# Kernel optimization log

Measured on AMD Instinct MI355X. Metric: run time of the kernel, lower is better.

## Reference

```python
import jax, jax.numpy as jnp
import numpy as np


def setup_inputs() -> dict:
    key = jax.random.key(0)
    k_idx, k_val = jax.random.split(key)
    XSIZE = 128
    N = 500000
    B = 16
    indices = jax.random.randint(k_idx, (N, 3), 0, XSIZE, dtype=jnp.int32)
    values = jax.random.normal(k_val, (B, N), dtype=jnp.float32)
    return {"indices": indices, "values": values, "xsize": XSIZE}


def reference(indices, values, xsize):
    # densitySmoothnessVolume: scatter-add values into a (B, X, X, X) grid,
    # then TV and MSE smoothness losses over 3-axis finite differences.
    B = values.shape[0]
    X = xsize
    # flat voxel index (z, y, x) -> z*X*X + y*X + x ; shared across batch
    flat = (indices[:, 0].astype(jnp.int32) * X + indices[:, 1]) * X + indices[:, 2]
    grid = jnp.zeros((B, X * X * X), dtype=values.dtype)
    grid = grid.at[:, flat].add(values)  # scatter-add, duplicate indices accumulate
    grid = grid.reshape(B, X, X, X)

    d1 = grid[:, 1:, :, :] - grid[:, :-1, :, :]
    d2 = grid[:, :, 1:, :] - grid[:, :, :-1, :]
    d3 = grid[:, :, :, 1:] - grid[:, :, :, :-1]

    axes = (1, 2, 3)
    # total variation loss, normalized by number of voxels X^3
    num_pixels = jnp.asarray(X * X * X, dtype=values.dtype)
    tv = (jnp.sum(jnp.abs(d1), axis=axes)
          + jnp.sum(jnp.abs(d2), axis=axes)
          + jnp.sum(jnp.abs(d3), axis=axes)) / num_pixels

    # MSE smoothness loss; normalizer replicates TF code exactly:
    # 2 * prod(shape[1:3]) - shape[1] - shape[2] = 2*X^2 - 2*X
    num_pixel_pairs = jnp.asarray(2 * X * X - 2 * X, dtype=values.dtype)
    mse = (jnp.sum(jnp.square(d1), axis=axes)
           + jnp.sum(jnp.square(d2), axis=axes)
           + jnp.sum(jnp.square(d3), axis=axes)) / num_pixel_pairs

    return jnp.stack([tv, mse])  # [2, B]
```

## Files before the change

kernel.cpp:

```cpp
#include <hip/hip_runtime.h>

#define XS 128
#define PLANE (XS * XS)
#define X3 (XS * XS * XS)
#define ZC 4
#define TPB 512
#define SLOTS 8
#define QPT 8

__device__ __forceinline__ void bar_lgkm() {
    __builtin_amdgcn_sched_barrier(0);
    asm volatile("s_waitcnt lgkmcnt(0)" ::: "memory");
    __builtin_amdgcn_s_barrier();
    __builtin_amdgcn_sched_barrier(0);
}

__global__ __launch_bounds__(256) void hist_kernel(
    const int* __restrict__ idx, int* __restrict__ hist, int N)
{
    __shared__ int lh[XS];
    for (int i = threadIdx.x; i < XS; i += 256) lh[i] = 0;
    __syncthreads();
    const int n4 = N >> 2;
    const int4* p = (const int4*)idx;
    for (int g = blockIdx.x * 256 + threadIdx.x; g < n4; g += gridDim.x * 256) {
        int4 A = p[3 * g], B = p[3 * g + 1], C = p[3 * g + 2];
        atomicAdd(&lh[A.x], 1); atomicAdd(&lh[A.w], 1);
        atomicAdd(&lh[B.z], 1); atomicAdd(&lh[C.y], 1);
    }
    for (int n = (n4 << 2) + blockIdx.x * 256 + threadIdx.x; n < N;
         n += gridDim.x * 256)
        atomicAdd(&lh[idx[3 * n]], 1);
    __syncthreads();
    for (int i = threadIdx.x; i < XS; i += 256)
        if (lh[i]) atomicAdd(&hist[i], lh[i]);
}

__global__ __launch_bounds__(128) void scan_kernel(
    const int* __restrict__ hist, int* __restrict__ base,
    int* __restrict__ cursor, float* __restrict__ out, int osz)
{
    __shared__ int sh[XS];
    const int t = threadIdx.x;
    const int h = hist[t];
    sh[t] = h;
    __syncthreads();
    for (int o = 1; o < XS; o <<= 1) {
        int v = (t >= o) ? sh[t - o] : 0;
        __syncthreads();
        sh[t] += v;
        __syncthreads();
    }
    const int excl = sh[t] - h;
    base[t] = excl; cursor[t] = excl;
    if (t < osz) out[t] = 0.f;
}

__global__ __launch_bounds__(256) void reorder_kernel(
    const int* __restrict__ idx, int* __restrict__ cursor,
    int2* __restrict__ list, int N)
{
    __shared__ int lh[XS], lbase[XS];
    const int c0 = blockIdx.x * 1024;
    int z[4], key[4], nn[4];
    int cntm = 0;

    for (int i = threadIdx.x; i < XS; i += 256) lh[i] = 0;

    if (c0 + 1024 <= N) {
        const int t = threadIdx.x;
        const int4* p = (const int4*)(idx + (size_t)c0 * 3);
        int4 A = p[3 * t], B = p[3 * t + 1], C = p[3 * t + 2];
        const int nb = c0 + 4 * t;
        z[0] = A.x; key[0] = (A.y << 7) | A.z; nn[0] = nb;
        z[1] = A.w; key[1] = (B.x << 7) | B.y; nn[1] = nb + 1;
        z[2] = B.z; key[2] = (B.w << 7) | C.x; nn[2] = nb + 2;
        z[3] = C.y; key[3] = (C.z << 7) | C.w; nn[3] = nb + 3;
        cntm = 4;
    } else {
        #pragma unroll
        for (int i = 0; i < 4; ++i) {
            const int n = c0 + 4 * threadIdx.x + i;
            if (n < N) {
                z[cntm]   = idx[3 * n];
                key[cntm] = (idx[3 * n + 1] << 7) | idx[3 * n + 2];
                nn[cntm]  = n;
                ++cntm;
            }
        }
    }
    __syncthreads();
    #pragma unroll
    for (int i = 0; i < 4; ++i)
        if (i < cntm) atomicAdd(&lh[z[i]], 1);
    __syncthreads();
    for (int i = threadIdx.x; i < XS; i += 256) {
        lbase[i] = lh[i] ? atomicAdd(&cursor[i], lh[i]) : 0;
        lh[i] = 0;
    }
    __syncthreads();
    #pragma unroll
    for (int i = 0; i < 4; ++i)
        if (i < cntm) {
            const int r = atomicAdd(&lh[z[i]], 1);
            list[lbase[z[i]] + r] = make_int2(nn[i], key[i]);
        }
}

__global__ __launch_bounds__(TPB, 4) void fused_kernel(
    const int2* __restrict__ list, const int* __restrict__ base,
    const int* __restrict__ cnt, const float* __restrict__ vals,
    float* __restrict__ out, int N, int Btot)
{
    __shared__ float buf[PLANE];
    __shared__ float rtv[TPB / 64], rms[TPB / 64];

    const int b   = blockIdx.x;
    const int z0  = blockIdx.y * ZC;
    const int tid = threadIdx.x;
    const float* vb = vals + (size_t)b * N;
    const int pmax = (z0 + ZC < XS) ? (z0 + ZC) : (XS - 1);

    int pos[SLOTS]; float val[SLOTS];
    int pc = 0, ps0 = 0;

    auto prefetch = [&](int zp) {
        ps0 = base[zp]; pc = cnt[zp];
        int2 e[SLOTS];
        #pragma unroll
        for (int i = 0; i < SLOTS; ++i) {
            const int ix = ps0 + tid + i * TPB;
            e[i] = list[ix < N ? ix : N - 1];
        }
        #pragma unroll
        for (int i = 0; i < SLOTS; ++i) { pos[i] = e[i].y; val[i] = vb[e[i].x]; }
    };
    auto scatter = [&]() {
        #pragma unroll
        for (int i = 0; i < SLOTS; ++i) {
            const float v = (tid + i * TPB < pc) ? val[i] : 0.f;
            atomicAdd(&buf[pos[i]], v);
        }
        for (int e = SLOTS * TPB + tid; e < pc; e += TPB) {
            const int2 en = list[ps0 + e];
            atomicAdd(&buf[en.y], vb[en.x]);
        }
    };

    prefetch(z0);
    #pragma unroll
    for (int i = 0; i < QPT; ++i)
        ((float4*)buf)[tid + i * TPB] = make_float4(0.f, 0.f, 0.f, 0.f);
    bar_lgkm();
    scatter();
    prefetch(z0 + 1);
    bar_lgkm();

    float4 prev[QPT];
    float tv = 0.f, ms = 0.f;

    for (int p = z0; p <= pmax; ++p) {
        float4 a[QPT];
        #pragma unroll
        for (int i = 0; i < QPT; ++i)
            a[i] = ((const float4*)buf)[tid + i * TPB];

        if (p > z0) {
            #pragma unroll
            for (int i = 0; i < QPT; ++i) {
                float d;
                d = a[i].x - prev[i].x; tv += fabsf(d); ms += d * d;
                d = a[i].y - prev[i].y; tv += fabsf(d); ms += d * d;
                d = a[i].z - prev[i].z; tv += fabsf(d); ms += d * d;
                d = a[i].w - prev[i].w; tv += fabsf(d); ms += d * d;
            }
        }
        if (p < z0 + ZC) {
            #pragma unroll
            for (int i = 0; i < QPT; ++i) {
                const int q = tid + i * TPB;
                const int qx = q & 31, y = q >> 5;
                float d;
                d = a[i].y - a[i].x; tv += fabsf(d); ms += d * d;
                d = a[i].z - a[i].y; tv += fabsf(d); ms += d * d;
                d = a[i].w - a[i].z; tv += fabsf(d); ms += d * d;
                if (qx < 31) {
                    d = buf[4 * q + 4] - a[i].w; tv += fabsf(d); ms += d * d;
                }
                if (y < XS - 1) {
                    const float4 u = ((const float4*)buf)[q + 32];
                    d = u.x - a[i].x; tv += fabsf(d); ms += d * d;
                    d = u.y - a[i].y; tv += fabsf(d); ms += d * d;
                    d = u.z - a[i].z; tv += fabsf(d); ms += d * d;
                    d = u.w - a[i].w; tv += fabsf(d); ms += d * d;
                }
            }
        }
        #pragma unroll
        for (int i = 0; i < QPT; ++i) prev[i] = a[i];

        if (p < pmax) {
            bar_lgkm();
            #pragma unroll
            for (int i = 0; i < QPT; ++i)
                ((float4*)buf)[tid + i * TPB] = make_float4(0.f, 0.f, 0.f, 0.f);
            bar_lgkm();
            scatter();
            if (p + 2 <= pmax) prefetch(p + 2);
            bar_lgkm();
        }
    }

    for (int o = 32; o > 0; o >>= 1) {
        tv += __shfl_down(tv, o); ms += __shfl_down(ms, o);
    }
    if ((tid & 63) == 0) { rtv[tid >> 6] = tv; rms[tid >> 6] = ms; }
    __syncthreads();
    if (tid == 0) {
        float t = 0.f, m = 0.f;
        #pragma unroll
        for (int w = 0; w < TPB / 64; ++w) { t += rtv[w]; m += rms[w]; }
        atomicAdd(out + b,        t * (1.0f / (float)X3));
        atomicAdd(out + Btot + b, m * (1.0f / (float)(2 * XS * XS - 2 * XS)));
    }
}

extern "C" void kernel_launch(void* const* d_in, const int* in_sizes, int n_in,
                              void* d_out, int out_size, void* d_ws, size_t ws_size,
                              hipStream_t stream)
{
    const int*   indices = (const int*)d_in[0];
    const float* values  = (const float*)d_in[1];
    const int N = in_sizes[0] / 3;
    const int B = in_sizes[1] / N;
    float* out = (float*)d_out;
    char*  ws  = (char*)d_ws;

    int2* list   = (int2*)ws;
    int*  hist   = (int*)(ws + (size_t)N * sizeof(int2));
    int*  basep  = hist + XS;
    int*  cursor = basep + XS;

    hipMemsetAsync(hist, 0, XS * sizeof(int), stream);
    hist_kernel<<<256, 256, 0, stream>>>(indices, hist, N);
    scan_kernel<<<1, 128, 0, stream>>>(hist, basep, cursor, out, out_size);
    reorder_kernel<<<(N + 1023) / 1024, 256, 0, stream>>>(
        indices, cursor, list, N);
    fused_kernel<<<dim3(B, XS / ZC), TPB, 0, stream>>>(
        list, basep, hist, values, out, N, B);
}
```

Before: 177.3 us.

## Pre-permute values into z-sorted layout so fused kernel reads coalesced

The reorder kernel now gathers all 16 batch values for each point and writes them into z-sorted slot order, followed by a new transpose kernel that produces a per-batch contiguous permuted value array. Positions are stored as 16-bit keys. The fused kernel then loads positions and values contiguously instead of making a dependent random gather through the point index. This trades extra passes and workspace traffic (two 16xN float arrays) for coalesced loads in the main kernel. The batch count is hardcoded to 16.

```diff
diff --git a/kernel.cpp b/kernel.cpp
--- a/kernel.cpp
+++ b/kernel.cpp
@@ -58,33 +58,33 @@
 
 __global__ __launch_bounds__(256) void reorder_kernel(
     const int* __restrict__ idx, int* __restrict__ cursor,
-    int2* __restrict__ list, int N)
+    const float* __restrict__ vals, float* __restrict__ pvT,
+    unsigned short* __restrict__ posArr, int N, int B)
 {
     __shared__ int lh[XS], lbase[XS];
     const int c0 = blockIdx.x * 1024;
-    int z[4], key[4], nn[4];
+    const int t = threadIdx.x;
+    int z[4], key[4];
     int cntm = 0;
-
-    for (int i = threadIdx.x; i < XS; i += 256) lh[i] = 0;
-
-    if (c0 + 1024 <= N) {
-        const int t = threadIdx.x;
+    const bool fast = (c0 + 1024 <= N);
+
+    for (int i = t; i < XS; i += 256) lh[i] = 0;
+
+    if (fast) {
         const int4* p = (const int4*)(idx + (size_t)c0 * 3);
-        int4 A = p[3 * t], B = p[3 * t + 1], C = p[3 * t + 2];
-        const int nb = c0 + 4 * t;
-        z[0] = A.x; key[0] = (A.y << 7) | A.z; nn[0] = nb;
-        z[1] = A.w; key[1] = (B.x << 7) | B.y; nn[1] = nb + 1;
-        z[2] = B.z; key[2] = (B.w << 7) | C.x; nn[2] = nb + 2;
-        z[3] = C.y; key[3] = (C.z << 7) | C.w; nn[3] = nb + 3;
+        int4 A = p[3 * t], B4 = p[3 * t + 1], C = p[3 * t + 2];
+        z[0] = A.x;  key[0] = (A.y << 7) | A.z;
+        z[1] = A.w;  key[1] = (B4.x << 7) | B4.y;
+        z[2] = B4.z; key[2] = (B4.w << 7) | C.x;
+        z[3] = C.y;  key[3] = (C.z << 7) | C.w;
         cntm = 4;
     } else {
         #pragma unroll
         for (int i = 0; i < 4; ++i) {
-            const int n = c0 + 4 * threadIdx.x + i;
+            const int n = c0 + 4 * t + i;
             if (n < N) {
                 z[cntm]   = idx[3 * n];
                 key[cntm] = (idx[3 * n + 1] << 7) | idx[3 * n + 2];
-                nn[cntm]  = n;
                 ++cntm;
             }
         }
@@ -94,22 +94,79 @@
     for (int i = 0; i < 4; ++i)
         if (i < cntm) atomicAdd(&lh[z[i]], 1);
     __syncthreads();
-    for (int i = threadIdx.x; i < XS; i += 256) {
+    for (int i = t; i < XS; i += 256) {
         lbase[i] = lh[i] ? atomicAdd(&cursor[i], lh[i]) : 0;
         lh[i] = 0;
     }
     __syncthreads();
+
+    int slot[4];
     #pragma unroll
     for (int i = 0; i < 4; ++i)
         if (i < cntm) {
             const int r = atomicAdd(&lh[z[i]], 1);
-            list[lbase[z[i]] + r] = make_int2(nn[i], key[i]);
-        }
+            slot[i] = lbase[z[i]] + r;
+            posArr[slot[i]] = (unsigned short)key[i];
+        }
+
+    if (fast) {
+        float4 vv[16];
+        #pragma unroll
+        for (int b = 0; b < 16; ++b)
+            vv[b] = *(const float4*)(vals + (size_t)b * N + c0 + 4 * t);
+        #pragma unroll
+        for (int i = 0; i < 4; ++i) {
+            float4* dst = (float4*)(pvT + (size_t)slot[i] * 16);
+            const float* s = (const float*)&vv[0];
+            float4 w0 = make_float4(((const float*)&vv[0])[i],  ((const float*)&vv[1])[i],
+                                    ((const float*)&vv[2])[i],  ((const float*)&vv[3])[i]);
+            float4 w1 = make_float4(((const float*)&vv[4])[i],  ((const float*)&vv[5])[i],
+                                    ((const float*)&vv[6])[i],  ((const float*)&vv[7])[i]);
+            float4 w2 = make_float4(((const float*)&vv[8])[i],  ((const float*)&vv[9])[i],
+                                    ((const float*)&vv[10])[i], ((const float*)&vv[11])[i]);
+            float4 w3 = make_float4(((const float*)&vv[12])[i], ((const float*)&vv[13])[i],
+                                    ((const float*)&vv[14])[i], ((const float*)&vv[15])[i]);
+            dst[0] = w0; dst[1] = w1; dst[2] = w2; dst[3] = w3;
+            (void)s;
+        }
+    } else {
+        for (int i = 0; i < cntm; ++i) {
+            const int n = c0 + 4 * t + i;
+            float* dst = pvT + (size_t)slot[i] * 16;
+            for (int b = 0; b < 16; ++b) dst[b] = vals[(size_t)b * N + n];
+        }
+    }
+}
+
+__global__ __launch_bounds__(256) void transpose_kernel(
+    const float4* __restrict__ pvT, float* __restrict__ pv, int N)
+{
+    __shared__ float tile[256][17];
+    const int t = threadIdx.x;
+    const int base = blockIdx.x * 256;
+
+    #pragma unroll
+    for (int i = 0; i < 4; ++i) {
+        const int f4 = t + i * 256;
+        const int s  = f4 >> 2;
+        if (base + s < N) {
+            float4 v = pvT[(size_t)base * 4 + f4];
+            const int c = (f4 & 3) * 4;
+            tile[s][c] = v.x; tile[s][c + 1] = v.y;
+            tile[s][c + 2] = v.z; tile[s][c + 3] = v.w;
+        }
+    }
+    __syncthreads();
+    if (base + t < N) {
+        #pragma unroll
+        for (int b = 0; b < 16; ++b)
+            pv[(size_t)b * N + base + t] = tile[t][b];
+    }
 }
 
 __global__ __launch_bounds__(TPB, 4) void fused_kernel(
-    const int2* __restrict__ list, const int* __restrict__ base,
-    const int* __restrict__ cnt, const float* __restrict__ vals,
+    const unsigned short* __restrict__ posArr, const int* __restrict__ base,
+    const int* __restrict__ cnt, const float* __restrict__ pv,
     float* __restrict__ out, int N, int Btot)
 {
     __shared__ float buf[PLANE];
@@ -118,7 +175,7 @@
     const int b   = blockIdx.x;
     const int z0  = blockIdx.y * ZC;
     const int tid = threadIdx.x;
-    const float* vb = vals + (size_t)b * N;
+    const float* pvb = pv + (size_t)b * N;
     const int pmax = (z0 + ZC < XS) ? (z0 + ZC) : (XS - 1);
 
     int pos[SLOTS]; float val[SLOTS];
@@ -126,14 +183,13 @@
 
     auto prefetch = [&](int zp) {
         ps0 = base[zp]; pc = cnt[zp];
-        int2 e[SLOTS];
         #pragma unroll
         for (int i = 0; i < SLOTS; ++i) {
             const int ix = ps0 + tid + i * TPB;
-            e[i] = list[ix < N ? ix : N - 1];
-        }
-        #pragma unroll
-        for (int i = 0; i < SLOTS; ++i) { pos[i] = e[i].y; val[i] = vb[e[i].x]; }
+            const int cx = ix < N ? ix : N - 1;
+            pos[i] = posArr[cx];
+            val[i] = pvb[cx];
+        }
     };
     auto scatter = [&]() {
         #pragma unroll
@@ -142,8 +198,7 @@
             atomicAdd(&buf[pos[i]], v);
         }
         for (int e = SLOTS * TPB + tid; e < pc; e += TPB) {
-            const int2 en = list[ps0 + e];
-            atomicAdd(&buf[en.y], vb[en.x]);
+            atomicAdd(&buf[posArr[ps0 + e]], pvb[ps0 + e]);
         }
     };
 
@@ -236,16 +291,22 @@
     float* out = (float*)d_out;
     char*  ws  = (char*)d_ws;
 
-    int2* list   = (int2*)ws;
-    int*  hist   = (int*)(ws + (size_t)N * sizeof(int2));
-    int*  basep  = hist + XS;
-    int*  cursor = basep + XS;
+    float* pvT = (float*)ws;
+    float* pv  = pvT + (size_t)16 * N;
+    unsigned short* posArr = (unsigned short*)(pv + (size_t)16 * N);
+    size_t poff = (size_t)32 * N * sizeof(float) + (size_t)N * sizeof(unsigned short);
+    poff = (poff + 255) & ~(size_t)255;
+    int* hist   = (int*)(ws + poff);
+    int* basep  = hist + XS;
+    int* cursor = basep + XS;
 
     hipMemsetAsync(hist, 0, XS * sizeof(int), stream);
     hist_kernel<<<256, 256, 0, stream>>>(indices, hist, N);
     scan_kernel<<<1, 128, 0, stream>>>(hist, basep, cursor, out, out_size);
     reorder_kernel<<<(N + 1023) / 1024, 256, 0, stream>>>(
-        indices, cursor, list, N);
+        indices, cursor, values, pvT, posArr, N, B);
+    transpose_kernel<<<(N + 255) / 256, 256, 0, stream>>>(
+        (const float4*)pvT, pv, N);
     fused_kernel<<<dim3(B, XS / ZC), TPB, 0, stream>>>(
-        list, basep, hist, values, out, N, B);
-}
+        posArr, basep, hist, pv, out, N, B);
+}
```

New measurement: 191.6 us. 8.1% more time.

## Replace histogram+scan with fixed-capacity per-plane buckets and use 1024-thread blocks

Applied to the files above, without the earlier changes.

Drops the histogram and prefix-scan kernels and the memset. Each z-plane instead gets a fixed-capacity bucket of CAP entries, and the reorder kernel's cursor counts serve directly as the per-plane counts. The fused kernel also moves from 512 to 1024 threads per block with fewer slots per thread. This saves two launches and a full read of the index array, but assumes no plane holds more than CAP entries. Prefetch reads past the valid count pick up garbage or uninitialised entries, which are clamped to keep them in bounds.

```diff
diff --git a/kernel.cpp b/kernel.cpp
--- a/kernel.cpp
+++ b/kernel.cpp
@@ -4,9 +4,10 @@
 #define PLANE (XS * XS)
 #define X3 (XS * XS * XS)
 #define ZC 4
-#define TPB 512
-#define SLOTS 8
-#define QPT 8
+#define TPB 1024
+#define SLOTS 4
+#define QPT 4
+#define CAP 8192
 
 __device__ __forceinline__ void bar_lgkm() {
     __builtin_amdgcn_sched_barrier(0);
@@ -15,44 +16,11 @@
     __builtin_amdgcn_sched_barrier(0);
 }
 
-__global__ __launch_bounds__(256) void hist_kernel(
-    const int* __restrict__ idx, int* __restrict__ hist, int N)
-{
-    __shared__ int lh[XS];
-    for (int i = threadIdx.x; i < XS; i += 256) lh[i] = 0;
-    __syncthreads();
-    const int n4 = N >> 2;
-    const int4* p = (const int4*)idx;
-    for (int g = blockIdx.x * 256 + threadIdx.x; g < n4; g += gridDim.x * 256) {
-        int4 A = p[3 * g], B = p[3 * g + 1], C = p[3 * g + 2];
-        atomicAdd(&lh[A.x], 1); atomicAdd(&lh[A.w], 1);
-        atomicAdd(&lh[B.z], 1); atomicAdd(&lh[C.y], 1);
-    }
-    for (int n = (n4 << 2) + blockIdx.x * 256 + threadIdx.x; n < N;
-         n += gridDim.x * 256)
-        atomicAdd(&lh[idx[3 * n]], 1);
-    __syncthreads();
-    for (int i = threadIdx.x; i < XS; i += 256)
-        if (lh[i]) atomicAdd(&hist[i], lh[i]);
-}
-
-__global__ __launch_bounds__(128) void scan_kernel(
-    const int* __restrict__ hist, int* __restrict__ base,
+__global__ __launch_bounds__(256) void init_kernel(
     int* __restrict__ cursor, float* __restrict__ out, int osz)
 {
-    __shared__ int sh[XS];
     const int t = threadIdx.x;
-    const int h = hist[t];
-    sh[t] = h;
-    __syncthreads();
-    for (int o = 1; o < XS; o <<= 1) {
-        int v = (t >= o) ? sh[t - o] : 0;
-        __syncthreads();
-        sh[t] += v;
-        __syncthreads();
-    }
-    const int excl = sh[t] - h;
-    base[t] = excl; cursor[t] = excl;
+    if (t < XS) cursor[t] = 0;
     if (t < osz) out[t] = 0.f;
 }
 
@@ -62,25 +30,25 @@
 {
     __shared__ int lh[XS], lbase[XS];
     const int c0 = blockIdx.x * 1024;
+    const int t = threadIdx.x;
     int z[4], key[4], nn[4];
     int cntm = 0;
 
-    for (int i = threadIdx.x; i < XS; i += 256) lh[i] = 0;
+    for (int i = t; i < XS; i += 256) lh[i] = 0;
 
     if (c0 + 1024 <= N) {
-        const int t = threadIdx.x;
         const int4* p = (const int4*)(idx + (size_t)c0 * 3);
-        int4 A = p[3 * t], B = p[3 * t + 1], C = p[3 * t + 2];
+        int4 A = p[3 * t], B4 = p[3 * t + 1], C = p[3 * t + 2];
         const int nb = c0 + 4 * t;
-        z[0] = A.x; key[0] = (A.y << 7) | A.z; nn[0] = nb;
-        z[1] = A.w; key[1] = (B.x << 7) | B.y; nn[1] = nb + 1;
-        z[2] = B.z; key[2] = (B.w << 7) | C.x; nn[2] = nb + 2;
-        z[3] = C.y; key[3] = (C.z << 7) | C.w; nn[3] = nb + 3;
+        z[0] = A.x;  key[0] = (A.y << 7) | A.z;   nn[0] = nb;
+        z[1] = A.w;  key[1] = (B4.x << 7) | B4.y; nn[1] = nb + 1;
+        z[2] = B4.z; key[2] = (B4.w << 7) | C.x;  nn[2] = nb + 2;
+        z[3] = C.y;  key[3] = (C.z << 7) | C.w;   nn[3] = nb + 3;
         cntm = 4;
     } else {
         #pragma unroll
         for (int i = 0; i < 4; ++i) {
-            const int n = c0 + 4 * threadIdx.x + i;
+            const int n = c0 + 4 * t + i;
             if (n < N) {
                 z[cntm]   = idx[3 * n];
                 key[cntm] = (idx[3 * n + 1] << 7) | idx[3 * n + 2];
@@ -94,7 +62,7 @@
     for (int i = 0; i < 4; ++i)
         if (i < cntm) atomicAdd(&lh[z[i]], 1);
     __syncthreads();
-    for (int i = threadIdx.x; i < XS; i += 256) {
+    for (int i = t; i < XS; i += 256) {
         lbase[i] = lh[i] ? atomicAdd(&cursor[i], lh[i]) : 0;
         lh[i] = 0;
     }
@@ -103,14 +71,14 @@
     for (int i = 0; i < 4; ++i)
         if (i < cntm) {
             const int r = atomicAdd(&lh[z[i]], 1);
-            list[lbase[z[i]] + r] = make_int2(nn[i], key[i]);
-        }
-}
-
-__global__ __launch_bounds__(TPB, 4) void fused_kernel(
-    const int2* __restrict__ list, const int* __restrict__ base,
-    const int* __restrict__ cnt, const float* __restrict__ vals,
-    float* __restrict__ out, int N, int Btot)
+            list[(size_t)z[i] * CAP + lbase[z[i]] + r] = make_int2(nn[i], key[i]);
+        }
+}
+
+__global__ __launch_bounds__(TPB, 8) void fused_kernel(
+    const int2* __restrict__ list, const int* __restrict__ cnt,
+    const float* __restrict__ vals, float* __restrict__ out,
+    int N, int Btot)
 {
     __shared__ float buf[PLANE];
     __shared__ float rtv[TPB / 64], rms[TPB / 64];
@@ -125,15 +93,17 @@
     int pc = 0, ps0 = 0;
 
     auto prefetch = [&](int zp) {
-        ps0 = base[zp]; pc = cnt[zp];
+        ps0 = zp * CAP; pc = cnt[zp];
         int2 e[SLOTS];
         #pragma unroll
+        for (int i = 0; i < SLOTS; ++i)
+            e[i] = list[(size_t)ps0 + tid + i * TPB];
+        #pragma unroll
         for (int i = 0; i < SLOTS; ++i) {
-            const int ix = ps0 + tid + i * TPB;
-            e[i] = list[ix < N ? ix : N - 1];
-        }
-        #pragma unroll
-        for (int i = 0; i < SLOTS; ++i) { pos[i] = e[i].y; val[i] = vb[e[i].x]; }
+            const unsigned nx = (unsigned)e[i].x < (unsigned)N ? e[i].x : 0u;
+            pos[i] = e[i].y & (PLANE - 1);
+            val[i] = vb[nx];
+        }
     };
     auto scatter = [&]() {
         #pragma unroll
@@ -142,7 +112,7 @@
             atomicAdd(&buf[pos[i]], v);
         }
         for (int e = SLOTS * TPB + tid; e < pc; e += TPB) {
-            const int2 en = list[ps0 + e];
+            const int2 en = list[(size_t)ps0 + e];
             atomicAdd(&buf[en.y], vb[en.x]);
         }
     };
@@ -237,15 +207,11 @@
     char*  ws  = (char*)d_ws;
 
     int2* list   = (int2*)ws;
-    int*  hist   = (int*)(ws + (size_t)N * sizeof(int2));
-    int*  basep  = hist + XS;
-    int*  cursor = basep + XS;
-
-    hipMemsetAsync(hist, 0, XS * sizeof(int), stream);
-    hist_kernel<<<256, 256, 0, stream>>>(indices, hist, N);
-    scan_kernel<<<1, 128, 0, stream>>>(hist, basep, cursor, out, out_size);
+    int*  cursor = (int*)(ws + (size_t)XS * CAP * sizeof(int2));
+
+    init_kernel<<<1, 256, 0, stream>>>(cursor, out, out_size);
     reorder_kernel<<<(N + 1023) / 1024, 256, 0, stream>>>(
         indices, cursor, list, N);
     fused_kernel<<<dim3(B, XS / ZC), TPB, 0, stream>>>(
-        list, basep, hist, values, out, N, B);
-}
+        list, cursor, values, out, N, B);
+}
```

After: 179.9 us. Within noise of the previous version (+1.5%).
